# Optimization experiments

Hardware: AMD Instinct MI355X
Metric: run time of the kernel (lower is better)

## Reference

```python
import jax, jax.numpy as jnp
import numpy as np

SI = 4   # input window size
SO = 2   # output sub-grid per window


def _compute_padding(dim, stride):
    if dim % stride == 0:
        return (0, 0)
    pad = (dim // stride + 1) * stride - dim
    return (pad // 2, pad - pad // 2)


def setup_inputs() -> dict:
    key = jax.random.key(0)
    k1, k2, k3 = jax.random.split(key, 3)
    x = jax.random.normal(k1, (16, 256, 128, 128), dtype=jnp.float32)
    w_key = jax.random.normal(k2, (64, 256), dtype=jnp.float32) * 0.05   # conv1x1 dim->key_dim
    w_sim = jax.random.normal(k3, (4, 64), dtype=jnp.float32) * 0.05     # conv1x1 key_dim->so^2
    return {"x": x, "w_key": w_key, "w_sim": w_sim}


def reference(x, w_key, w_sim):
    si, so = SI, SO
    N, C, H, W = x.shape
    pad_t, pad_b = _compute_padding(H, si)
    pad_l, pad_r = _compute_padding(W, si)
    x = jnp.pad(x, ((0, 0), (0, 0), (pad_t, pad_b), (pad_l, pad_r)))
    N, C, H, W = x.shape
    h, w = H // si, W // si
    so2, si2 = so * so, si * si

    # 1x1 convs: key = relu(Wk x), kq = Ws key
    key = jax.nn.relu(jnp.einsum('nchw,kc->nkhw', x, w_key))
    kq = jnp.einsum('nkhw,sk->nshw', key, w_sim)              # [N, so^2, H, W]

    # windowize: [N, C, h, w, si*si] -> [N, h, w, C, si*si]
    xw = x.reshape(N, C, h, si, w, si).transpose(0, 2, 4, 1, 3, 5).reshape(N, h, w, C, si2)
    # kq windows: [N, h, w, si*si, so^2]
    kqw = kq.reshape(N, so2, h, si, w, si).transpose(0, 2, 4, 3, 5, 1).reshape(N, h, w, si2, so2)
    kqw = jax.nn.softmax(kqw / si, axis=3)

    # per-window softmax-weighted aggregation: [N,h,w,C,so^2]
    out = jnp.einsum('nhwcp,nhwpq->nhwcq', xw, kqw)
    out = out.reshape(N, h, w, C, so, so).transpose(0, 3, 1, 4, 2, 5)
    return out.reshape(N, C, h * so, w * so)
```

## Files before the change

kernel.cpp:

```cpp
#include <hip/hip_runtime.h>
#include <cstdint>


#define CIN 256

typedef __attribute__((ext_vector_type(8))) short short8;
typedef __attribute__((ext_vector_type(4))) float floatx4;

__device__ __forceinline__ short f2bf(float f) {
    union { float f; uint32_t u; } v; v.f = f;
    uint32_t u = v.u + 0x7fffu + ((v.u >> 16) & 1u);
    return (short)(u >> 16);
}

__global__ void cvt_wkey_kernel(const float* __restrict__ wk,
                                short* __restrict__ wkb) {
    int i = blockIdx.x * 256 + threadIdx.x;
    wkb[i] = f2bf(wk[i]);
}

__global__ __launch_bounds__(256) void fds_kernel(
    const float* __restrict__ x, const short* __restrict__ wkb,
    const float* __restrict__ wsim, float* __restrict__ out)
{
    __shared__ float xs[16][260];
    __shared__ float keyS[16][68];
    __shared__ float kqL[64];
    __shared__ float wgtS[64];

    const int b   = blockIdx.x;
    const int wid = (b & 7) * 2048 + (b >> 3);
    const int n   = wid >> 10;
    const int hh  = (wid >> 5) & 31;
    const int ww  = wid & 31;

    const int t = threadIdx.x;

    {
        const int c = t;
        const float* xb = x + (((size_t)(n * CIN + c) * 128 + hh * 4) * 128 + ww * 4);
        #pragma unroll
        for (int r = 0; r < 4; ++r) {
            float4 v = *(const float4*)(xb + (size_t)r * 128);
            xs[r * 4 + 0][c] = v.x;
            xs[r * 4 + 1][c] = v.y;
            xs[r * 4 + 2][c] = v.z;
            xs[r * 4 + 3][c] = v.w;
        }
    }
    __syncthreads();

    {
        const int l    = t & 63;
        const int wv   = t >> 6;
        const int mrow = l & 15;
        const int kq8  = (l >> 4) * 8;
        floatx4 acc = {0.f, 0.f, 0.f, 0.f};
        #pragma unroll
        for (int ks = 0; ks < 8; ++ks) {
            const float* ap = &xs[mrow][ks * 32 + kq8];
            short8 af;
            #pragma unroll
            for (int j = 0; j < 8; ++j) af[j] = f2bf(ap[j]);
            short8 bfr = *(const short8*)(wkb + ((wv * 16 + mrow) * 256 + ks * 32 + kq8));
            acc = __builtin_amdgcn_mfma_f32_16x16x32_bf16(af, bfr, acc, 0, 0, 0);
        }
        #pragma unroll
        for (int r = 0; r < 4; ++r) {
            const int p = (l >> 4) * 4 + r;
            keyS[p][wv * 16 + mrow] = fmaxf(acc[r], 0.f);
        }
    }
    __syncthreads();

    if (t < 64) {
        const int p = t >> 2, s = t & 3;
        float acc = 0.f;
        #pragma unroll 8
        for (int k = 0; k < 64; ++k) acc += keyS[p][k] * wsim[s * 64 + k];
        kqL[t] = acc * 0.25f;
    }
    __syncthreads();

    if (t < 64) {
        const int s = t & 3;
        float m = -1e30f;
        #pragma unroll
        for (int p2 = 0; p2 < 16; ++p2) m = fmaxf(m, kqL[p2 * 4 + s]);
        float sum = 0.f;
        #pragma unroll
        for (int p2 = 0; p2 < 16; ++p2) sum += __expf(kqL[p2 * 4 + s] - m);
        wgtS[t] = __expf(kqL[t] - m) / sum;
    }
    __syncthreads();

    {
        const int c = t;
        float a0 = 0.f, a1 = 0.f, a2 = 0.f, a3 = 0.f;
        #pragma unroll
        for (int p = 0; p < 16; ++p) {
            const float xv = xs[p][c];
            a0 += xv * wgtS[p * 4 + 0];
            a1 += xv * wgtS[p * 4 + 1];
            a2 += xv * wgtS[p * 4 + 2];
            a3 += xv * wgtS[p * 4 + 3];
        }
        float* ob = out + (((size_t)(n * CIN + c) * 64 + hh * 2) * 64 + ww * 2);
        *(float2*)(ob)      = make_float2(a0, a1);
        *(float2*)(ob + 64) = make_float2(a2, a3);
    }
}

extern "C" void kernel_launch(void* const* d_in, const int* in_sizes, int n_in,
                              void* d_out, int out_size, void* d_ws, size_t ws_size,
                              hipStream_t stream) {
    const float* x    = (const float*)d_in[0];
    const float* wkey = (const float*)d_in[1];
    const float* wsim = (const float*)d_in[2];
    float* out = (float*)d_out;
    short* wkb = (short*)d_ws;

    cvt_wkey_kernel<<<64, 256, 0, stream>>>(wkey, wkb);
    fds_kernel<<<16384, 256, 0, stream>>>(x, wkb, wsim, out);
}
```

Measured before the change: 465.7 us.

## Keep window in registers, stage bf16 in LDS, parallelize kq and softmax

Result: faster. 449.1 us (-3.6%).

```diff
diff --git a/kernel.cpp b/kernel.cpp
--- a/kernel.cpp
+++ b/kernel.cpp
@@ -7,25 +7,29 @@
 typedef __attribute__((ext_vector_type(8))) short short8;
 typedef __attribute__((ext_vector_type(4))) float floatx4;
 
-__device__ __forceinline__ short f2bf(float f) {
+__device__ __forceinline__ short f2bf_rn(float f) {
     union { float f; uint32_t u; } v; v.f = f;
     uint32_t u = v.u + 0x7fffu + ((v.u >> 16) & 1u);
     return (short)(u >> 16);
+}
+__device__ __forceinline__ short f2bf_rh(float f) {
+    union { float f; uint32_t u; } v; v.f = f;
+    return (short)((v.u + 0x8000u) >> 16);
 }
 
 __global__ void cvt_wkey_kernel(const float* __restrict__ wk,
                                 short* __restrict__ wkb) {
     int i = blockIdx.x * 256 + threadIdx.x;
-    wkb[i] = f2bf(wk[i]);
+    wkb[i] = f2bf_rn(wk[i]);
 }
 
-__global__ __launch_bounds__(256) void fds_kernel(
+__global__ __launch_bounds__(256, 8) void fds_kernel(
     const float* __restrict__ x, const short* __restrict__ wkb,
     const float* __restrict__ wsim, float* __restrict__ out)
 {
-    __shared__ float xs[16][260];
+    __shared__ short xs[16][264];
     __shared__ float keyS[16][68];
-    __shared__ float kqL[64];
+    __shared__ float partS[256];
     __shared__ float wgtS[64];
 
     const int b   = blockIdx.x;
@@ -33,20 +37,21 @@
     const int n   = wid >> 10;
     const int hh  = (wid >> 5) & 31;
     const int ww  = wid & 31;
+    const int t   = threadIdx.x;
 
-    const int t = threadIdx.x;
-
+    float v[16];
     {
-        const int c = t;
-        const float* xb = x + (((size_t)(n * CIN + c) * 128 + hh * 4) * 128 + ww * 4);
+        const float* xb = x + (((size_t)(n * CIN + t) * 128 + hh * 4) * 128 + ww * 4);
+        float4 r0 = *(const float4*)(xb);
+        float4 r1 = *(const float4*)(xb + 128);
+        float4 r2 = *(const float4*)(xb + 256);
+        float4 r3 = *(const float4*)(xb + 384);
+        v[0]=r0.x;  v[1]=r0.y;  v[2]=r0.z;  v[3]=r0.w;
+        v[4]=r1.x;  v[5]=r1.y;  v[6]=r1.z;  v[7]=r1.w;
+        v[8]=r2.x;  v[9]=r2.y;  v[10]=r2.z; v[11]=r2.w;
+        v[12]=r3.x; v[13]=r3.y; v[14]=r3.z; v[15]=r3.w;
         #pragma unroll
-        for (int r = 0; r < 4; ++r) {
-            float4 v = *(const float4*)(xb + (size_t)r * 128);
-            xs[r * 4 + 0][c] = v.x;
-            xs[r * 4 + 1][c] = v.y;
-            xs[r * 4 + 2][c] = v.z;
-            xs[r * 4 + 3][c] = v.w;
-        }
+        for (int p = 0; p < 16; ++p) xs[p][t] = f2bf_rh(v[p]);
     }
     __syncthreads();
 
@@ -58,54 +63,61 @@
         floatx4 acc = {0.f, 0.f, 0.f, 0.f};
         #pragma unroll
         for (int ks = 0; ks < 8; ++ks) {
-            const float* ap = &xs[mrow][ks * 32 + kq8];
-            short8 af;
-            #pragma unroll
-            for (int j = 0; j < 8; ++j) af[j] = f2bf(ap[j]);
+            short8 af  = *(const short8*)(&xs[mrow][ks * 32 + kq8]);
             short8 bfr = *(const short8*)(wkb + ((wv * 16 + mrow) * 256 + ks * 32 + kq8));
             acc = __builtin_amdgcn_mfma_f32_16x16x32_bf16(af, bfr, acc, 0, 0, 0);
         }
         #pragma unroll
-        for (int r = 0; r < 4; ++r) {
-            const int p = (l >> 4) * 4 + r;
-            keyS[p][wv * 16 + mrow] = fmaxf(acc[r], 0.f);
+        for (int r = 0; r < 4; ++r)
+            keyS[(l >> 4) * 4 + r][wv * 16 + mrow] = fmaxf(acc[r], 0.f);
+    }
+    __syncthreads();
+
+    {
+        const int p  = t >> 4;
+        const int s  = (t >> 2) & 3;
+        const int kk = t & 3;
+        const float4* kp = (const float4*)&keyS[p][kk * 16];
+        const float4* wp = (const float4*)(wsim + s * 64 + kk * 16);
+        float acc = 0.f;
+        #pragma unroll
+        for (int j = 0; j < 4; ++j) {
+            float4 kj = kp[j];
+            float4 wj = wp[j];
+            acc += kj.x * wj.x + kj.y * wj.y + kj.z * wj.z + kj.w * wj.w;
         }
+        partS[t] = acc;
     }
     __syncthreads();
 
     if (t < 64) {
         const int p = t >> 2, s = t & 3;
-        float acc = 0.f;
-        #pragma unroll 8
-        for (int k = 0; k < 64; ++k) acc += keyS[p][k] * wsim[s * 64 + k];
-        kqL[t] = acc * 0.25f;
-    }
-    __syncthreads();
-
-    if (t < 64) {
-        const int s = t & 3;
-        float m = -1e30f;
+        float4 pr = *(const float4*)&partS[p * 16 + s * 4];
+        float logit = 0.25f * (pr.x + pr.y + pr.z + pr.w);
+        float m = logit;
         #pragma unroll
-        for (int p2 = 0; p2 < 16; ++p2) m = fmaxf(m, kqL[p2 * 4 + s]);
-        float sum = 0.f;
+        for (int msk = 4; msk < 64; msk <<= 1)
+            m = fmaxf(m, __shfl_xor(m, msk, 64));
+        float e = __expf(logit - m);
+        float ssum = e;
         #pragma unroll
-        for (int p2 = 0; p2 < 16; ++p2) sum += __expf(kqL[p2 * 4 + s] - m);
-        wgtS[t] = __expf(kqL[t] - m) / sum;
+        for (int msk = 4; msk < 64; msk <<= 1)
+            ssum += __shfl_xor(ssum, msk, 64);
+        wgtS[t] = e / ssum;
     }
     __syncthreads();
 
     {
-        const int c = t;
         float a0 = 0.f, a1 = 0.f, a2 = 0.f, a3 = 0.f;
         #pragma unroll
         for (int p = 0; p < 16; ++p) {
-            const float xv = xs[p][c];
-            a0 += xv * wgtS[p * 4 + 0];
-            a1 += xv * wgtS[p * 4 + 1];
-            a2 += xv * wgtS[p * 4 + 2];
-            a3 += xv * wgtS[p * 4 + 3];
+            float4 wq = *(const float4*)&wgtS[p * 4];
+            a0 += v[p] * wq.x;
+            a1 += v[p] * wq.y;
+            a2 += v[p] * wq.z;
+            a3 += v[p] * wq.w;
         }
-        float* ob = out + (((size_t)(n * CIN + c) * 64 + hh * 2) * 64 + ww * 2);
+        float* ob = out + (((size_t)(n * CIN + t) * 64 + hh * 2) * 64 + ww * 2);
         *(float2*)(ob)      = make_float2(a0, a1);
         *(float2*)(ob + 64) = make_float2(a2, a3);
     }
```
